# Kernel optimization log

Measured on AMD Instinct MI355X. Metric: run time of the kernel, lower is better.

## Reference

```python
import jax, jax.numpy as jnp
import numpy as np

B_, L_, H_, P_ = 8, 4096, 512, 256
DT_MIN, DT_MAX = 1e-3, 1e-1


def setup_inputs() -> dict:
    key = jax.random.key(0)
    ks = jax.random.split(key, 6)
    input_sequence = jax.random.normal(ks[0], (B_, L_, H_), jnp.float32)
    # Stable diagonal SSM eigenvalues (HiPPO-like): negative real, spread imaginary
    Lambda_re = -0.5 * jnp.ones((P_,), jnp.float32)
    Lambda_im = jnp.pi * jnp.arange(P_, dtype=jnp.float32)
    # B, C stored as real arrays with trailing real/imag channel, as in the module
    B = jax.random.normal(ks[1], (P_, H_, 2), jnp.float32) / np.sqrt(2.0 * H_)
    C = jax.random.normal(ks[2], (H_, P_, 2), jnp.float32) / np.sqrt(float(P_))
    D = jax.random.normal(ks[3], (H_,), jnp.float32)
    log_step = jax.random.uniform(ks[4], (P_,), jnp.float32,
                                  float(np.log(DT_MIN)), float(np.log(DT_MAX)))
    return dict(input_sequence=input_sequence, Lambda_re=Lambda_re,
                Lambda_im=Lambda_im, B=B, C=C, D=D, log_step=log_step)


def _scan_ssm(Lambda_bar, Bu):
    """Diagonal linear recurrence x_k = Lambda_bar * x_{k-1} + Bu_k via parallel scan.
    Lambda_bar: (P,) complex64; Bu: (L, P) complex64 -> xs: (L, P) complex64."""
    A = jnp.broadcast_to(Lambda_bar, Bu.shape)

    def binop(e_i, e_j):
        a_i, b_i = e_i
        a_j, b_j = e_j
        return a_j * a_i, a_j * b_i + b_j

    _, xs = jax.lax.associative_scan(binop, (A, Bu))
    return xs


def reference(input_sequence, Lambda_re, Lambda_im, B, C, D, log_step):
    # complex parameters (conj_sym=True, clip_eigs=False, zoh discretization)
    Lambda = (Lambda_re + 1j * Lambda_im).astype(jnp.complex64)        # (P,)
    B_tilde = (B[..., 0] + 1j * B[..., 1]).astype(jnp.complex64)       # (P, H)
    C_tilde = (C[..., 0] + 1j * C[..., 1]).astype(jnp.complex64)       # (H, P)
    step = jnp.exp(log_step)                                           # (P,)
    # ZOH: Lambda_bar = exp(Lambda*dt); B_bar = Lambda^{-1}(Lambda_bar - I) B
    Lambda_bar = jnp.exp(Lambda * step)                                # (P,)
    B_bar = ((1.0 / Lambda) * (Lambda_bar - 1.0))[:, None] * B_tilde   # (P, H)
    # project inputs into state space: (B, L, P)
    Bu = jnp.einsum('blh,ph->blp', input_sequence.astype(jnp.complex64), B_bar)
    xs = jax.vmap(lambda bu: _scan_ssm(Lambda_bar, bu))(Bu)            # (B, L, P)
    state = xs[:, -1, :]                                               # (B, P)
    # conj_sym=True -> output uses 2 * Re(C x)
    ys = 2.0 * jnp.einsum('blp,hp->blh', xs, C_tilde).real             # (B, L, H)
    out = ys + D * input_sequence                                      # D-skip
    return out, state
```

## Files before the change

kernel.cpp:

```cpp
#include <hip/hip_runtime.h>
#include <hip/hip_bf16.h>

#define Hh 512
#define Pp 256
#define Ll 4096
#define Bb 8
#define BL (Bb*Ll)
#define Sc 64
#define NC 64

typedef __attribute__((ext_vector_type(8))) __bf16 bf16x8;
typedef __attribute__((ext_vector_type(4))) float  floatx4;

#define LAM_OFF     0
#define LAMS64D_OFF 512
#define B1G_OFF     1024
#define B3G_OFF     (B1G_OFF + 65536)
#define UB16_OFF    (B3G_OFF + 65536)
#define BUB_OFF     (UB16_OFF + 4194304)
#define XSB_OFF     (BUB_OFF + 4194304)
#define AGG_OFF     (XSB_OFF + 4194304)

#define OUT_ELEMS 16777216

#define GLL16(g, l) __builtin_amdgcn_global_load_lds( \
    (const __attribute__((address_space(1))) void*)(g), \
    (__attribute__((address_space(3))) void*)(l), 16, 0, 0)

#define BAR_LGKM()  asm volatile("s_waitcnt lgkmcnt(0)\n\ts_barrier" ::: "memory")
#define BAR_VMN(n)  asm volatile("s_waitcnt vmcnt(" #n ")\n\ts_barrier" ::: "memory")

__device__ __forceinline__ float2 cmul(float2 a, float2 b) {
    return make_float2(a.x*b.x - a.y*b.y, a.x*b.y + a.y*b.x);
}
__device__ __forceinline__ void cfma(float2& acc, float2 a, float2 b) {
    acc.x = fmaf(a.x, b.x, acc.x); acc.x = fmaf(-a.y, b.y, acc.x);
    acc.y = fmaf(a.x, b.y, acc.y); acc.y = fmaf( a.y, b.x, acc.y);
}

__global__ void prep(const float* __restrict__ u,
                     const float* __restrict__ Bmat, const float* __restrict__ Cmat,
                     const float* __restrict__ Lre, const float* __restrict__ Lim,
                     const float* __restrict__ logstep, float2* __restrict__ ws) {
    int bid = blockIdx.x;
    if (bid < 8192) {
        long i = ((long)bid * 256 + threadIdx.x) * 8;
        float4 v0 = *(const float4*)(u + i);
        float4 v1 = *(const float4*)(u + i + 4);
        __align__(16) __hip_bfloat162 t[4];
        t[0] = __float22bfloat162_rn(make_float2(v0.x, v0.y));
        t[1] = __float22bfloat162_rn(make_float2(v0.z, v0.w));
        t[2] = __float22bfloat162_rn(make_float2(v1.x, v1.y));
        t[3] = __float22bfloat162_rn(make_float2(v1.z, v1.w));
        *(bf16x8*)((__hip_bfloat16*)(ws + UB16_OFF) + i) = *(const bf16x8*)t;
    } else if (bid < 8704) {
        int idx = (bid - 8192) * 256 + threadIdx.x;
        int p = idx >> 9, h = idx & 511;
        double lr = (double)Lre[p], li = (double)Lim[p];
        double st = exp((double)logstep[p]);
        double a  = lr * st, th = li * st;
        double er = exp(a);
        double lamr = er * cos(th), lami = er * sin(th);
        double nr = lamr - 1.0, ni = lami;
        double den = lr*lr + li*li;
        float gx = (float)((nr*lr + ni*li)/den), gy = (float)((ni*lr - nr*li)/den);
        float2 b = ((const float2*)Bmat)[idx];
        float re = gx*b.x - gy*b.y;
        float im = gx*b.y + gy*b.x;
        __hip_bfloat16* B1 = (__hip_bfloat16*)(ws + B1G_OFF);
        B1[(2*p)*512 + h]   = __float2bfloat16(re);
        B1[(2*p+1)*512 + h] = __float2bfloat16(im);
    } else if (bid < 9216) {
        int idx = (bid - 8704) * 256 + threadIdx.x;
        int h = idx >> 8, p = idx & 255;
        float2 c = ((const float2*)Cmat)[idx];
        __hip_bfloat162* B3 = (__hip_bfloat162*)(ws + B3G_OFF);
        B3[h*256 + p] = __float22bfloat162_rn(make_float2(2.f*c.x, -2.f*c.y));
    } else {
        int p = threadIdx.x;
        double lr = (double)Lre[p], li = (double)Lim[p];
        double st = exp((double)logstep[p]);
        double a  = lr * st, th = li * st;
        double er = exp(a);
        ws[LAM_OFF + p] = make_float2((float)(er*cos(th)), (float)(er*sin(th)));
        double er64 = exp(64.0 * a), th64 = 64.0 * th;
        ((double2*)(ws + LAMS64D_OFF))[p] = make_double2(er64*cos(th64), er64*sin(th64));
    }
}

#define STAGE(buf, kt) do { \
    _Pragma("unroll") \
    for (int h_ = 0; h_ < 2; ++h_) { \
        _Pragma("unroll") \
        for (int r_ = 0; r_ < 2; ++r_) { \
            GLL16(aSrc + (h_*128 + r_*64)*1024 + (kt)*128, \
                  ldsSt + (buf)*65536 + h_*16384 + r_*8192); \
            GLL16(bSrc + (h_*128 + r_*64)*1024 + (kt)*128, \
                  ldsSt + (buf)*65536 + 32768 + h_*16384 + r_*8192); \
        } \
    } \
} while (0)

template<int EPI>
__global__ __launch_bounds__(512, 2)
void gemm8(const __hip_bfloat16* __restrict__ A,
           const __hip_bfloat16* __restrict__ B,
           void* __restrict__ Cout,
           const __hip_bfloat16* __restrict__ ub,
           const float* __restrict__ Dv,
           const float2* __restrict__ lamTab,
           float2* __restrict__ aggOut) {
    __shared__ __align__(16) char lds[131072];
    const int tid = threadIdx.x;
    const int w = tid >> 6, l = tid & 63;

    const int idx = blockIdx.x;
    const int swz = (idx & 7) * 32 + (idx >> 3);
    const int mt = swz >> 1, nt = swz & 1;
    const long M0 = (long)mt * 256;
    const int  N0 = nt * 256;

    const int rA  = l >> 3;
    const int csw = ((l & 7) ^ rA) * 16;
    const char* aSrc = (const char*)A + (M0 + w*8 + rA) * 1024 + csw;
    const char* bSrc = (const char*)B + (long)(N0 + w*8 + rA) * 1024 + csw;
    char* ldsSt = lds + w*1024 + l*16;

    const int quad = l >> 4, ml = l & 15, m7 = ml & 7;
    const int wm = w & 1, wn = w >> 1;
    const int o0 = ((quad    ) ^ m7) * 16;
    const int o1 = ((quad + 4) ^ m7) * 16;
    const char* aRd = lds + wm*16384 + ml*128;
    const char* bRd = lds + 32768 + (wn >> 1)*16384 + ((wn & 1)*64 + ml)*128;

    floatx4 acc[8][4];
    #pragma unroll
    for (int i = 0; i < 8; ++i)
        #pragma unroll
        for (int j = 0; j < 4; ++j) acc[i][j] = (floatx4)0.f;

    STAGE(0, 0);
    STAGE(1, 1);
    BAR_VMN(8);

    #pragma unroll
    for (int t = 0; t < 8; ++t) {
        const int tb = (t & 1) * 65536;

        {
            bf16x8 af[8], bfr[4];
            #pragma unroll
            for (int fm = 0; fm < 8; ++fm)
                af[fm] = *(const bf16x8*)(aRd + tb + fm*2048 + o0);
            #pragma unroll
            for (int fn = 0; fn < 4; ++fn)
                bfr[fn] = *(const bf16x8*)(bRd + tb + fn*2048 + o0);
            __builtin_amdgcn_s_setprio(1);
            #pragma unroll
            for (int fm = 0; fm < 8; ++fm)
                #pragma unroll
                for (int fn = 0; fn < 4; ++fn)
                    acc[fm][fn] = __builtin_amdgcn_mfma_f32_16x16x32_bf16(
                        af[fm], bfr[fn], acc[fm][fn], 0, 0, 0);
            __builtin_amdgcn_s_setprio(0);
        }

        {
            bf16x8 af[8], bfr[4];
            #pragma unroll
            for (int fm = 0; fm < 8; ++fm)
                af[fm] = *(const bf16x8*)(aRd + tb + fm*2048 + o1);
            #pragma unroll
            for (int fn = 0; fn < 4; ++fn)
                bfr[fn] = *(const bf16x8*)(bRd + tb + fn*2048 + o1);
            BAR_LGKM();
            if (t + 2 < 8) STAGE(t & 1, t + 2);
            __builtin_amdgcn_sched_barrier(0);
            __builtin_amdgcn_s_setprio(1);
            #pragma unroll
            for (int fm = 0; fm < 8; ++fm)
                #pragma unroll
                for (int fn = 0; fn < 4; ++fn)
                    acc[fm][fn] = __builtin_amdgcn_mfma_f32_16x16x32_bf16(
                        af[fm], bfr[fn], acc[fm][fn], 0, 0, 0);
            __builtin_amdgcn_s_setprio(0);
        }

        if (t < 6)       BAR_VMN(8);
        else if (t == 6) BAR_VMN(0);
    }

    if constexpr (EPI == 0) {
        const int b   = (int)(M0 >> 12);
        const int gc0 = (int)((M0 >> 6) & 63);
        #pragma unroll
        for (int fn = 0; fn < 4; ++fn) {
            const int col = N0 + wn*64 + fn*16 + ml;
            const int p = col >> 1;
            const float2 lam = lamTab[p];
            const float2 one = make_float2(1.f, 0.f);
            const float2 l2  = cmul(lam, lam);
            const float2 l3  = cmul(l2, lam);
            const float2 l4  = cmul(l2, l2);
            const float2 l8  = cmul(l4, l4);
            const float2 l12 = cmul(l8, l4);
            const float2 l16 = cmul(l8, l8);
            const float2 l32 = cmul(l16, l16);
            const float2 l48 = cmul(l32, l16);
            const float2 P4q = (quad==3) ? one : (quad==2) ? l4 : (quad==1) ? l8 : l12;
            #pragma unroll
            for (int c = 0; c < 2; ++c) {
                float2 sc = make_float2(0.f, 0.f);
                #pragma unroll
                for (int a = 0; a < 4; ++a) {
                    const int fm = c*4 + a;
                    float vr[4];
                    #pragma unroll
                    for (int reg = 0; reg < 4; ++reg) {
                        const long row = M0 + wm*128 + fm*16 + quad*4 + reg;
                        __hip_bfloat16 hv = __float2bfloat16(acc[fm][fn][reg]);
                        ((__hip_bfloat16*)Cout)[row * 512 + col] = hv;
                        vr[reg] = __bfloat162float(hv);
                    }
                    float2 s;
                    s.x = fmaf(l3.x, vr[0], fmaf(l2.x, vr[1], fmaf(lam.x, vr[2], vr[3])));
                    s.y = fmaf(l3.y, vr[0], fmaf(l2.y, vr[1], lam.y * vr[2]));
                    const float2 p16 = (a==3) ? one : (a==2) ? l16 : (a==1) ? l32 : l48;
                    cfma(sc, cmul(p16, P4q), s);
                }
                sc.x += __shfl_xor(sc.x, 16); sc.y += __shfl_xor(sc.y, 16);
                sc.x += __shfl_xor(sc.x, 32); sc.y += __shfl_xor(sc.y, 32);
                const float ox = __shfl_xor(sc.x, 1);
                const float oy = __shfl_xor(sc.y, 1);
                if (quad == 0 && (ml & 1) == 0) {
                    aggOut[(b*NC + gc0 + wm*2 + c) * Pp + p] =
                        make_float2(sc.x - oy, sc.y + ox);
                }
            }
        }
    } else {
        #pragma unroll
        for (int fm = 0; fm < 8; ++fm)
            #pragma unroll
            for (int fn = 0; fn < 4; ++fn) {
                const int col = N0 + wn*64 + fn*16 + ml;
                const float d = Dv[col];
                #pragma unroll
                for (int reg = 0; reg < 4; ++reg) {
                    const long row = M0 + wm*128 + fm*16 + quad*4 + reg;
                    const long o = row * 512 + col;
                    ((float*)Cout)[o] = acc[fm][fn][reg] + d * __bfloat162float(ub[o]);
                }
            }
    }
}

__global__ void k2c(float2* __restrict__ ws, float* __restrict__ dout) {
    int p = threadIdx.x;
    int bc = blockIdx.x;
    int b = bc >> 6, c = bc & 63;
    float2 lam = ws[LAM_OFF + p];
    double2 l64 = ((const double2*)(ws + LAMS64D_OFF))[p];
    double cr = 0.0, ci = 0.0;
    for (int cp = 0; cp < c; ++cp) {
        float2 a = ws[AGG_OFF + (b*NC + cp) * Pp + p];
        double nr = fma(l64.x, cr, (double)a.x); nr = fma(-l64.y, ci, nr);
        double ni = fma(l64.x, ci, (double)a.y); ni = fma( l64.y, cr, ni);
        cr = nr; ci = ni;
    }
    float2 x = make_float2((float)cr, (float)ci);
    const __hip_bfloat162* __restrict__ bub = (const __hip_bfloat162*)(ws + BUB_OFF);
    __hip_bfloat162* __restrict__ xsb = (__hip_bfloat162*)(ws + XSB_OFF);
    long base = (long)(b*Ll + c*Sc) * Pp + p;
    for (int j0 = 0; j0 < Sc; j0 += 8) {
        float2 v[8];
        #pragma unroll
        for (int i = 0; i < 8; ++i)
            v[i] = __bfloat1622float2(bub[base + (long)(j0 + i) * Pp]);
        #pragma unroll
        for (int i = 0; i < 8; ++i) {
            float nr = fmaf(lam.x, x.x, v[i].x); nr = fmaf(-lam.y, x.y, nr);
            float ni = fmaf(lam.x, x.y, v[i].y); ni = fmaf( lam.y, x.x, ni);
            x.x = nr; x.y = ni;
            xsb[base + (long)(j0 + i) * Pp] = __float22bfloat162_rn(make_float2(x.x, x.y));
        }
    }
    if (c == NC - 1) {
        dout[OUT_ELEMS + b * Pp + p] = x.x;
        dout[OUT_ELEMS + Bb * Pp + b * Pp + p] = x.y;
    }
}

extern "C" void kernel_launch(void* const* d_in, const int* in_sizes, int n_in,
                              void* d_out, int out_size, void* d_ws, size_t ws_size,
                              hipStream_t stream) {
    const float* u       = (const float*)d_in[0];
    const float* Lre     = (const float*)d_in[1];
    const float* Lim     = (const float*)d_in[2];
    const float* Bmat    = (const float*)d_in[3];
    const float* Cmat    = (const float*)d_in[4];
    const float* Dv      = (const float*)d_in[5];
    const float* logstep = (const float*)d_in[6];
    float*  out = (float*)d_out;
    float2* ws  = (float2*)d_ws;

    prep<<<9217, 256, 0, stream>>>(u, Bmat, Cmat, Lre, Lim, logstep, ws);

    gemm8<0><<<256, 512, 0, stream>>>(
        (const __hip_bfloat16*)(ws + UB16_OFF),
        (const __hip_bfloat16*)(ws + B1G_OFF),
        (void*)(ws + BUB_OFF), nullptr, nullptr,
        (const float2*)(ws + LAM_OFF), (float2*)(ws + AGG_OFF));

    k2c<<<Bb*NC, 256, 0, stream>>>(ws, out);

    gemm8<1><<<256, 512, 0, stream>>>(
        (const __hip_bfloat16*)(ws + XSB_OFF),
        (const __hip_bfloat16*)(ws + B3G_OFF),
        (void*)out,
        (const __hip_bfloat16*)(ws + UB16_OFF), Dv,
        nullptr, nullptr);
}
```

Before: 205.6 us.

## Fuse chunk scan into second GEMM, generating A tiles in LDS

Removes the separate k2c scan kernel and the xs bf16 round-trip through global memory. The second GEMM now computes the chunk carries from the aggregates, runs the intra-chunk recurrence on 128 threads per K-tile, and writes the bf16 states straight into swizzled LDS as the A operand. In exchange the GEMM mainloop is serialized behind a scalar scan on a quarter of the threads, with more barriers and a larger LDS footprint. Each block also redoes the carry prefix over up to 63 chunks.

```diff
diff --git a/kernel.cpp b/kernel.cpp
--- a/kernel.cpp
+++ b/kernel.cpp
@@ -101,13 +101,10 @@
     } \
 } while (0)
 
-template<int EPI>
 __global__ __launch_bounds__(512, 2)
-void gemm8(const __hip_bfloat16* __restrict__ A,
+void gemm1(const __hip_bfloat16* __restrict__ A,
            const __hip_bfloat16* __restrict__ B,
            void* __restrict__ Cout,
-           const __hip_bfloat16* __restrict__ ub,
-           const float* __restrict__ Dv,
            const float2* __restrict__ lamTab,
            float2* __restrict__ aggOut) {
     __shared__ __align__(16) char lds[131072];
@@ -131,7 +128,7 @@
     const int o0 = ((quad    ) ^ m7) * 16;
     const int o1 = ((quad + 4) ^ m7) * 16;
     const char* aRd = lds + wm*16384 + ml*128;
-    const char* bRd = lds + 32768 + (wn >> 1)*16384 + ((wn & 1)*64 + ml)*128;
+    const char* bRd = lds + 32768 + wn*8192 + ml*128;
 
     floatx4 acc[8][4];
     #pragma unroll
@@ -146,7 +143,6 @@
     #pragma unroll
     for (int t = 0; t < 8; ++t) {
         const int tb = (t & 1) * 65536;
-
         {
             bf16x8 af[8], bfr[4];
             #pragma unroll
@@ -164,7 +160,6 @@
                         af[fm], bfr[fn], acc[fm][fn], 0, 0, 0);
             __builtin_amdgcn_s_setprio(0);
         }
-
         {
             bf16x8 af[8], bfr[4];
             #pragma unroll
@@ -185,110 +180,218 @@
                         af[fm], bfr[fn], acc[fm][fn], 0, 0, 0);
             __builtin_amdgcn_s_setprio(0);
         }
-
         if (t < 6)       BAR_VMN(8);
         else if (t == 6) BAR_VMN(0);
     }
 
-    if constexpr (EPI == 0) {
-        const int b   = (int)(M0 >> 12);
-        const int gc0 = (int)((M0 >> 6) & 63);
-        #pragma unroll
-        for (int fn = 0; fn < 4; ++fn) {
-            const int col = N0 + wn*64 + fn*16 + ml;
-            const int p = col >> 1;
-            const float2 lam = lamTab[p];
-            const float2 one = make_float2(1.f, 0.f);
-            const float2 l2  = cmul(lam, lam);
-            const float2 l3  = cmul(l2, lam);
-            const float2 l4  = cmul(l2, l2);
-            const float2 l8  = cmul(l4, l4);
-            const float2 l12 = cmul(l8, l4);
-            const float2 l16 = cmul(l8, l8);
-            const float2 l32 = cmul(l16, l16);
-            const float2 l48 = cmul(l32, l16);
-            const float2 P4q = (quad==3) ? one : (quad==2) ? l4 : (quad==1) ? l8 : l12;
-            #pragma unroll
-            for (int c = 0; c < 2; ++c) {
-                float2 sc = make_float2(0.f, 0.f);
-                #pragma unroll
-                for (int a = 0; a < 4; ++a) {
-                    const int fm = c*4 + a;
-                    float vr[4];
-                    #pragma unroll
-                    for (int reg = 0; reg < 4; ++reg) {
-                        const long row = M0 + wm*128 + fm*16 + quad*4 + reg;
-                        __hip_bfloat16 hv = __float2bfloat16(acc[fm][fn][reg]);
-                        ((__hip_bfloat16*)Cout)[row * 512 + col] = hv;
-                        vr[reg] = __bfloat162float(hv);
-                    }
-                    float2 s;
-                    s.x = fmaf(l3.x, vr[0], fmaf(l2.x, vr[1], fmaf(lam.x, vr[2], vr[3])));
-                    s.y = fmaf(l3.y, vr[0], fmaf(l2.y, vr[1], lam.y * vr[2]));
-                    const float2 p16 = (a==3) ? one : (a==2) ? l16 : (a==1) ? l32 : l48;
-                    cfma(sc, cmul(p16, P4q), s);
-                }
-                sc.x += __shfl_xor(sc.x, 16); sc.y += __shfl_xor(sc.y, 16);
-                sc.x += __shfl_xor(sc.x, 32); sc.y += __shfl_xor(sc.y, 32);
-                const float ox = __shfl_xor(sc.x, 1);
-                const float oy = __shfl_xor(sc.y, 1);
-                if (quad == 0 && (ml & 1) == 0) {
-                    aggOut[(b*NC + gc0 + wm*2 + c) * Pp + p] =
-                        make_float2(sc.x - oy, sc.y + ox);
-                }
-            }
-        }
-    } else {
-        #pragma unroll
-        for (int fm = 0; fm < 8; ++fm)
-            #pragma unroll
-            for (int fn = 0; fn < 4; ++fn) {
-                const int col = N0 + wn*64 + fn*16 + ml;
-                const float d = Dv[col];
+    const int b   = (int)(M0 >> 12);
+    const int gc0 = (int)((M0 >> 6) & 63);
+    #pragma unroll
+    for (int fn = 0; fn < 4; ++fn) {
+        const int col = N0 + wn*64 + fn*16 + ml;
+        const int p = col >> 1;
+        const float2 lam = lamTab[p];
+        const float2 one = make_float2(1.f, 0.f);
+        const float2 l2  = cmul(lam, lam);
+        const float2 l3  = cmul(l2, lam);
+        const float2 l4  = cmul(l2, l2);
+        const float2 l8  = cmul(l4, l4);
+        const float2 l12 = cmul(l8, l4);
+        const float2 l16 = cmul(l8, l8);
+        const float2 l32 = cmul(l16, l16);
+        const float2 l48 = cmul(l32, l16);
+        const float2 P4q = (quad==3) ? one : (quad==2) ? l4 : (quad==1) ? l8 : l12;
+        #pragma unroll
+        for (int c = 0; c < 2; ++c) {
+            float2 sc = make_float2(0.f, 0.f);
+            #pragma unroll
+            for (int a = 0; a < 4; ++a) {
+                const int fm = c*4 + a;
+                float vr[4];
                 #pragma unroll
                 for (int reg = 0; reg < 4; ++reg) {
                     const long row = M0 + wm*128 + fm*16 + quad*4 + reg;
-                    const long o = row * 512 + col;
-                    ((float*)Cout)[o] = acc[fm][fn][reg] + d * __bfloat162float(ub[o]);
+                    __hip_bfloat16 hv = __float2bfloat16(acc[fm][fn][reg]);
+                    ((__hip_bfloat16*)Cout)[row * 512 + col] = hv;
+                    vr[reg] = __bfloat162float(hv);
+                }
+                float2 s;
+                s.x = fmaf(l3.x, vr[0], fmaf(l2.x, vr[1], fmaf(lam.x, vr[2], vr[3])));
+                s.y = fmaf(l3.y, vr[0], fmaf(l2.y, vr[1], lam.y * vr[2]));
+                const float2 p16 = (a==3) ? one : (a==2) ? l16 : (a==1) ? l32 : l48;
+                cfma(sc, cmul(p16, P4q), s);
+            }
+            sc.x += __shfl_xor(sc.x, 16); sc.y += __shfl_xor(sc.y, 16);
+            sc.x += __shfl_xor(sc.x, 32); sc.y += __shfl_xor(sc.y, 32);
+            const float ox = __shfl_xor(sc.x, 1);
+            const float oy = __shfl_xor(sc.y, 1);
+            if (quad == 0 && (ml & 1) == 0) {
+                aggOut[(b*NC + gc0 + wm*2 + c) * Pp + p] =
+                    make_float2(sc.x - oy, sc.y + ox);
+            }
+        }
+    }
+}
+
+#define STAGEB(buf, kt) do { \
+    _Pragma("unroll") \
+    for (int h_ = 0; h_ < 2; ++h_) { \
+        _Pragma("unroll") \
+        for (int r_ = 0; r_ < 2; ++r_) { \
+            GLL16(bSrc + (h_*128 + r_*64)*1024 + (kt)*128, \
+                  ldsB + (buf)*32768 + h_*16384 + r_*8192); \
+        } \
+    } \
+} while (0)
+
+__global__ __launch_bounds__(512, 2)
+void gemm2f(const __hip_bfloat162* __restrict__ bub,
+            const __hip_bfloat16* __restrict__ Bg,
+            float* __restrict__ out,
+            const __hip_bfloat16* __restrict__ ub,
+            const float* __restrict__ Dv,
+            const float2* __restrict__ lamTab,
+            const double2* __restrict__ lam64,
+            const float2* __restrict__ agg) {
+    __shared__ __align__(16) char lds[139264];
+    const int tid = threadIdx.x;
+    const int w = tid >> 6, l = tid & 63;
+
+    const int idx = blockIdx.x;
+    const int swz = (idx & 7) * 32 + (idx >> 3);
+    const int mt = swz >> 1, nt = swz & 1;
+    const long M0 = (long)mt * 256;
+    const int  N0 = nt * 256;
+    const int b   = (int)(M0 >> 12);
+    const int gc0 = (int)((M0 >> 6) & 63);
+
+    const int rA  = l >> 3;
+    const int csw = ((l & 7) ^ rA) * 16;
+    const char* bSrc = (const char*)Bg + (long)(N0 + w*8 + rA) * 1024 + csw;
+    char* ldsB = lds + 65536 + w*1024 + l*16;
+
+    const int quad = l >> 4, ml = l & 15, m7 = ml & 7;
+    const int wm = w & 1, wn = w >> 1;
+    const int o0 = ((quad    ) ^ m7) * 16;
+    const int o1 = ((quad + 4) ^ m7) * 16;
+    const char* aRd = lds + wm*16384 + ml*128;
+    const char* bRd = lds + 65536 + wn*8192 + ml*128;
+
+    float2* carryL = (float2*)(lds + 131072);
+
+    if (tid < 256) {
+        const int p = tid;
+        const double2 l64 = lam64[p];
+        double cr = 0.0, ci = 0.0;
+        for (int cp = 0; cp < gc0; ++cp) {
+            float2 a = agg[(b*NC + cp) * Pp + p];
+            double nr = fma(l64.x, cr, (double)a.x); nr = fma(-l64.y, ci, nr);
+            double ni = fma(l64.x, ci, (double)a.y); ni = fma( l64.y, cr, ni);
+            cr = nr; ci = ni;
+        }
+        carryL[0*256 + p] = make_float2((float)cr, (float)ci);
+        #pragma unroll
+        for (int i = 1; i < 4; ++i) {
+            float2 a = agg[(b*NC + gc0 + i - 1) * Pp + p];
+            double nr = fma(l64.x, cr, (double)a.x); nr = fma(-l64.y, ci, nr);
+            double ni = fma(l64.x, ci, (double)a.y); ni = fma( l64.y, cr, ni);
+            cr = nr; ci = ni;
+            carryL[i*256 + p] = make_float2((float)cr, (float)ci);
+        }
+    }
+    __syncthreads();
+
+    floatx4 acc[8][4];
+    #pragma unroll
+    for (int i = 0; i < 8; ++i)
+        #pragma unroll
+        for (int j = 0; j < 4; ++j) acc[i][j] = (floatx4)0.f;
+
+    auto scanTile = [&](int kt, int bufA) {
+        if (tid < 128) {
+            const int p5 = tid & 31, chunk = tid >> 5;
+            const int p = kt*32 + p5;
+            const float2 lam = lamTab[p];
+            float2 x = carryL[chunk*256 + p];
+            const __hip_bfloat162* src = bub + ((long)(M0 + chunk*64)) * 256 + p;
+            char* abase = lds + bufA*32768 + (chunk*64)*128;
+            const int cs = p5*4;
+            for (int j0 = 0; j0 < 64; j0 += 8) {
+                float2 v[8];
+                #pragma unroll
+                for (int i = 0; i < 8; ++i)
+                    v[i] = __bfloat1622float2(src[(long)(j0 + i) * 256]);
+                #pragma unroll
+                for (int i = 0; i < 8; ++i) {
+                    float nr = fmaf(lam.x, x.x, v[i].x); nr = fmaf(-lam.y, x.y, nr);
+                    float ni = fmaf(lam.x, x.y, v[i].y); ni = fmaf( lam.y, x.x, ni);
+                    x.x = nr; x.y = ni;
+                    const int j = j0 + i;
+                    *(__hip_bfloat162*)(abase + j*128 + (cs ^ ((j & 7) << 4))) =
+                        __float22bfloat162_rn(x);
                 }
             }
+            if (gc0 == 60 && chunk == 3 && nt == 0) {
+                out[OUT_ELEMS + b * Pp + p] = x.x;
+                out[OUT_ELEMS + Bb * Pp + b * Pp + p] = x.y;
+            }
+        }
+    };
+
+    scanTile(0, 0);
+    STAGEB(0, 0);
+    __syncthreads();
+
+    for (int kt = 0; kt < 8; ++kt) {
+        const int cb = kt & 1;
+        if (kt < 7) { scanTile(kt + 1, cb ^ 1); STAGEB(cb ^ 1, kt + 1); }
+        __syncthreads();
+        const int tb = cb * 32768;
+        bf16x8 af[8], bfr[4];
+        #pragma unroll
+        for (int fm = 0; fm < 8; ++fm)
+            af[fm] = *(const bf16x8*)(aRd + tb + fm*2048 + o0);
+        #pragma unroll
+        for (int fn = 0; fn < 4; ++fn)
+            bfr[fn] = *(const bf16x8*)(bRd + tb + fn*2048 + o0);
+        __builtin_amdgcn_s_setprio(1);
+        #pragma unroll
+        for (int fm = 0; fm < 8; ++fm)
+            #pragma unroll
+            for (int fn = 0; fn < 4; ++fn)
+                acc[fm][fn] = __builtin_amdgcn_mfma_f32_16x16x32_bf16(
+                    af[fm], bfr[fn], acc[fm][fn], 0, 0, 0);
+        __builtin_amdgcn_s_setprio(0);
+        #pragma unroll
+        for (int fm = 0; fm < 8; ++fm)
+            af[fm] = *(const bf16x8*)(aRd + tb + fm*2048 + o1);
+        #pragma unroll
+        for (int fn = 0; fn < 4; ++fn)
+            bfr[fn] = *(const bf16x8*)(bRd + tb + fn*2048 + o1);
+        __builtin_amdgcn_s_setprio(1);
+        #pragma unroll
+        for (int fm = 0; fm < 8; ++fm)
+            #pragma unroll
+            for (int fn = 0; fn < 4; ++fn)
+                acc[fm][fn] = __builtin_amdgcn_mfma_f32_16x16x32_bf16(
+                    af[fm], bfr[fn], acc[fm][fn], 0, 0, 0);
+        __builtin_amdgcn_s_setprio(0);
+        __syncthreads();
     }
-}
-
-__global__ void k2c(float2* __restrict__ ws, float* __restrict__ dout) {
-    int p = threadIdx.x;
-    int bc = blockIdx.x;
-    int b = bc >> 6, c = bc & 63;
-    float2 lam = ws[LAM_OFF + p];
-    double2 l64 = ((const double2*)(ws + LAMS64D_OFF))[p];
-    double cr = 0.0, ci = 0.0;
-    for (int cp = 0; cp < c; ++cp) {
-        float2 a = ws[AGG_OFF + (b*NC + cp) * Pp + p];
-        double nr = fma(l64.x, cr, (double)a.x); nr = fma(-l64.y, ci, nr);
-        double ni = fma(l64.x, ci, (double)a.y); ni = fma( l64.y, cr, ni);
-        cr = nr; ci = ni;
-    }
-    float2 x = make_float2((float)cr, (float)ci);
-    const __hip_bfloat162* __restrict__ bub = (const __hip_bfloat162*)(ws + BUB_OFF);
-    __hip_bfloat162* __restrict__ xsb = (__hip_bfloat162*)(ws + XSB_OFF);
-    long base = (long)(b*Ll + c*Sc) * Pp + p;
-    for (int j0 = 0; j0 < Sc; j0 += 8) {
-        float2 v[8];
-        #pragma unroll
-        for (int i = 0; i < 8; ++i)
-            v[i] = __bfloat1622float2(bub[base + (long)(j0 + i) * Pp]);
-        #pragma unroll
-        for (int i = 0; i < 8; ++i) {
-            float nr = fmaf(lam.x, x.x, v[i].x); nr = fmaf(-lam.y, x.y, nr);
-            float ni = fmaf(lam.x, x.y, v[i].y); ni = fmaf( lam.y, x.x, ni);
-            x.x = nr; x.y = ni;
-            xsb[base + (long)(j0 + i) * Pp] = __float22bfloat162_rn(make_float2(x.x, x.y));
-        }
-    }
-    if (c == NC - 1) {
-        dout[OUT_ELEMS + b * Pp + p] = x.x;
-        dout[OUT_ELEMS + Bb * Pp + b * Pp + p] = x.y;
-    }
+
+    #pragma unroll
+    for (int fm = 0; fm < 8; ++fm)
+        #pragma unroll
+        for (int fn = 0; fn < 4; ++fn) {
+            const int col = N0 + wn*64 + fn*16 + ml;
+            const float d = Dv[col];
+            #pragma unroll
+            for (int reg = 0; reg < 4; ++reg) {
+                const long row = M0 + wm*128 + fm*16 + quad*4 + reg;
+                const long o = row * 512 + col;
+                out[o] = acc[fm][fn][reg] + d * __bfloat162float(ub[o]);
+            }
+        }
 }
 
 extern "C" void kernel_launch(void* const* d_in, const int* in_sizes, int n_in,
@@ -306,18 +409,18 @@
 
     prep<<<9217, 256, 0, stream>>>(u, Bmat, Cmat, Lre, Lim, logstep, ws);
 
-    gemm8<0><<<256, 512, 0, stream>>>(
+    gemm1<<<256, 512, 0, stream>>>(
         (const __hip_bfloat16*)(ws + UB16_OFF),
         (const __hip_bfloat16*)(ws + B1G_OFF),
-        (void*)(ws + BUB_OFF), nullptr, nullptr,
+        (void*)(ws + BUB_OFF),
         (const float2*)(ws + LAM_OFF), (float2*)(ws + AGG_OFF));
 
-    k2c<<<Bb*NC, 256, 0, stream>>>(ws, out);
-
-    gemm8<1><<<256, 512, 0, stream>>>(
-        (const __hip_bfloat16*)(ws + XSB_OFF),
+    gemm2f<<<256, 512, 0, stream>>>(
+        (const __hip_bfloat162*)(ws + BUB_OFF),
         (const __hip_bfloat16*)(ws + B3G_OFF),
-        (void*)out,
+        out,
         (const __hip_bfloat16*)(ws + UB16_OFF), Dv,
-        nullptr, nullptr);
-}
+        (const float2*)(ws + LAM_OFF),
+        (const double2*)(ws + LAMS64D_OFF),
+        (const float2*)(ws + AGG_OFF));
+}
```

Result: faster. 196.6 us (-4.4%).
